# Performance work log

Hardware: AMD Instinct MI355X
Metric: run time of the kernel (lower is better)

The kernel has to match this reference:

```python
import jax, jax.numpy as jnp
import numpy as np

HEADS = 8
DIM_HEAD = 64
SCALE = DIM_HEAD ** -0.5
POS_DIM = 64


def _sincos_pe(H, W, dim, dtype):
    # matches build_2d_sincos_pos_embed: [1, dim, H, W]
    y = jnp.linspace(-1.0, 1.0, H)[:, None] * jnp.ones((1, W), jnp.float32)
    x = jnp.ones((H, 1), jnp.float32) * jnp.linspace(-1.0, 1.0, W)[None, :]
    omega = 1.0 / (10000.0 ** (jnp.arange(dim // 4, dtype=jnp.float32) / (dim // 4)))
    px = x[..., None] * omega  # [H, W, dim//4]
    py = y[..., None] * omega
    pe = jnp.concatenate([jnp.sin(px), jnp.cos(px), jnp.sin(py), jnp.cos(py)], axis=-1)
    return pe.transpose(2, 0, 1)[None].astype(dtype)


def _conv2d(x, w):
    return jax.lax.conv_general_dilated(
        x, w, (1, 1), 'SAME', dimension_numbers=('NCHW', 'OIHW', 'NCHW'))


def _sobel(d):
    kx = jnp.array([[1, 0, -1], [2, 0, -2], [1, 0, -1]], jnp.float32).reshape(1, 1, 3, 3)
    ky = jnp.array([[1, 2, 1], [0, 0, 0], [-1, -2, -1]], jnp.float32).reshape(1, 1, 3, 3)
    return _conv2d(d, kx), _conv2d(d, ky)


def setup_inputs() -> dict:
    key = jax.random.key(0)
    ks = jax.random.split(key, 8)
    B, C, H, W = 2, 256, 64, 64
    hid = HEADS * DIM_HEAD  # 512
    s = 0.02
    return {
        'x': jax.random.normal(ks[0], (B, C, H, W), jnp.float32),
        'dsm': jax.random.uniform(ks[1], (B, 1, H, W), jnp.float32),
        'wq': jax.random.normal(ks[2], (hid, C), jnp.float32) * s,
        'wkv': jax.random.normal(ks[3], (2 * hid, C + 1), jnp.float32) * s,
        'wout': jax.random.normal(ks[4], (C, hid), jnp.float32) * s,
        'bout': jnp.zeros((C,), jnp.float32),
        'w_hape': jax.random.normal(ks[5], (hid, POS_DIM + 3), jnp.float32) * s,
        'b_hape': jnp.zeros((hid,), jnp.float32),
        'w_alpha': jax.random.normal(ks[6], (1, 1, 3, 3), jnp.float32) * 0.1,
        'b_alpha': jnp.zeros((1,), jnp.float32),
    }


def reference(x, dsm, wq, wkv, wout, bout, w_hape, b_hape, w_alpha, b_alpha):
    B, C, H, W = x.shape
    hid = wq.shape[0]
    # per-sample min-max normalize DSM over spatial dims
    dmin = dsm.min(axis=(2, 3), keepdims=True)
    dmax = dsm.max(axis=(2, 3), keepdims=True)
    d = (dsm - dmin) / (dmax - dmin + 1e-6)
    # HAPE: [PE | h | grad_h] -> 1x1 conv to hidden
    pe = jnp.broadcast_to(_sincos_pe(H, W, POS_DIM, x.dtype), (B, POS_DIM, H, W))
    gx, gy = _sobel(d)
    hape_in = jnp.concatenate([pe, d, gx, gy], axis=1)  # [B, 67, H, W]
    hape_k = jnp.einsum('oc,bchw->bohw', w_hape, hape_in) + b_hape[None, :, None, None]
    # QKV via 1x1 convs
    q = jnp.einsum('oc,bchw->bohw', wq, x)
    kv = jnp.einsum('oc,bchw->bohw', wkv, jnp.concatenate([x, d], axis=1))
    k = kv[:, :hid] + hape_k
    v = kv[:, hid:]
    to_heads = lambda t: t.reshape(B, HEADS, DIM_HEAD, H * W)  # b (h c) x y -> b h c (xy)
    qh = to_heads(q) * SCALE
    kh = to_heads(k)
    vh = to_heads(v)
    sim = jnp.einsum('bhdi,bhdj->bhij', qh, kh)  # [B, h, N, N]
    attn = jax.nn.softmax(sim, axis=-1)
    out = jnp.einsum('bhij,bhdj->bhid', attn, vh)  # [B, h, N, d]
    # b h (x y) d -> b (h d) x y
    out = out.transpose(0, 1, 3, 2).reshape(B, HEADS * DIM_HEAD, H, W)
    out = jnp.einsum('oc,bchw->bohw', wout, out) + bout[None, :, None, None]
    # fine: gradient-magnitude alpha gating
    mag = jnp.sqrt(jnp.maximum(gx, 0.0) ** 2 + jnp.maximum(gy, 0.0) ** 2 + 1e-12)
    alpha = jax.nn.sigmoid(_conv2d(mag, w_alpha) + b_alpha[None, :, None, None])
    return x + out * alpha
```

## Files before the change

### kernel.cpp

```cpp
#include <hip/hip_runtime.h>
#include <math.h>

#define NPOS 4096
#define MTOT 8192
#define KP   352
#define HT 64
#define WT 64
#define NSPLIT 2
#define KEYS_PER (NPOS / NSPLIT)
#define NCH (KEYS_PER / 64)


typedef unsigned short ushortT;
typedef short v8s __attribute__((ext_vector_type(8)));
typedef float v4f __attribute__((ext_vector_type(4)));
typedef unsigned uint2v __attribute__((ext_vector_type(2)));

static __device__ __forceinline__ ushortT bfr(float f) {
    union { float f; unsigned u; } v; v.f = f;
    return (ushortT)((v.u + 0x8000u) >> 16);
}
static __device__ __forceinline__ unsigned pack2bf(float a, float b) {
    union { float f; unsigned u; } ua, ub; ua.f = a; ub.f = b;
    return __builtin_amdgcn_perm(ub.u + 0x8000u, ua.u + 0x8000u, 0x07060302u);
}
static __device__ __forceinline__ unsigned pack2bf_t(float a, float b) {
    union { float f; unsigned u; } ua, ub; ua.f = a; ub.f = b;
    return __builtin_amdgcn_perm(ub.u, ua.u, 0x07060302u);
}
static __device__ __forceinline__ float fexp2(float x) {
#if __has_builtin(__builtin_amdgcn_exp2f)
    return __builtin_amdgcn_exp2f(x);
#else
    return exp2f(x);
#endif
}
static __device__ __forceinline__ float bflo(unsigned u) {
    union { unsigned u; float f; } v; v.u = u << 16; return v.f;
}
static __device__ __forceinline__ float bfhi(unsigned u) {
    union { unsigned u; float f; } v; v.u = u & 0xffff0000u; return v.f;
}

__global__ void k_pre(const float* __restrict__ dsm,
                      const float* __restrict__ walpha, const float* __restrict__ balpha,
                      const float* __restrict__ x,
                      const float* __restrict__ wq, const float* __restrict__ wkv,
                      const float* __restrict__ whape, const float* __restrict__ bhape,
                      const float* __restrict__ wout,
                      ushortT* __restrict__ F, float* __restrict__ alpha,
                      ushortT* __restrict__ Wc, float* __restrict__ biasc,
                      ushortT* __restrict__ woutb) {
    __shared__ __align__(16) ushortT Tl[64][72];
    __shared__ float smn[4], smx[4];
    int role = blockIdx.x;
    int t = threadIdx.x;

    if (role < 32) {
        int idx = role * 256 + t;
        int b = idx / NPOS, n = idx % NPOS;
        int hh = n / WT, ww = n % WT;
        const float* dp = dsm + (size_t)b * NPOS;

        float mn = 1e30f, mx = -1e30f;
        for (int i = t; i < NPOS; i += 256) {
            float v = dp[i];
            mn = fminf(mn, v); mx = fmaxf(mx, v);
        }
        for (int off = 32; off; off >>= 1) {
            mn = fminf(mn, __shfl_xor(mn, off, 64));
            mx = fmaxf(mx, __shfl_xor(mx, off, 64));
        }
        int wid = t >> 6;
        if ((t & 63) == 0) { smn[wid] = mn; smx[wid] = mx; }
        __syncthreads();
        float dmin = fminf(fminf(smn[0], smn[1]), fminf(smn[2], smn[3]));
        float dmax = fmaxf(fmaxf(smx[0], smx[1]), fmaxf(smx[2], smx[3]));
        float inv = 1.0f / (dmax - dmin + 1e-6f);

        float dwin[5][5];
        #pragma unroll
        for (int dy = 0; dy < 5; dy++)
            #pragma unroll
            for (int dx = 0; dx < 5; dx++) {
                int y = hh + dy - 2, xx = ww + dx - 2;
                float v = 0.0f;
                if (y >= 0 && y < HT && xx >= 0 && xx < WT) v = (dp[y * WT + xx] - dmin) * inv;
                dwin[dy][dx] = v;
            }

        float gxc = 0.f, gyc = 0.f, conv = 0.f;
        #pragma unroll
        for (int oy = 0; oy < 3; oy++)
            #pragma unroll
            for (int ox = 0; ox < 3; ox++) {
                int qy = hh + oy - 1, qx = ww + ox - 1;
                float m = 0.0f;
                if (qy >= 0 && qy < HT && qx >= 0 && qx < WT) {
                    float gx = dwin[oy][ox] - dwin[oy][ox + 2]
                             + 2.f * dwin[oy + 1][ox] - 2.f * dwin[oy + 1][ox + 2]
                             + dwin[oy + 2][ox] - dwin[oy + 2][ox + 2];
                    float gy = dwin[oy][ox] + 2.f * dwin[oy][ox + 1] + dwin[oy][ox + 2]
                             - dwin[oy + 2][ox] - 2.f * dwin[oy + 2][ox + 1] - dwin[oy + 2][ox + 2];
                    if (oy == 1 && ox == 1) { gxc = gx; gyc = gy; }
                    float rx = fmaxf(gx, 0.f), ry = fmaxf(gy, 0.f);
                    m = sqrtf(rx * rx + ry * ry + 1e-12f);
                }
                conv += walpha[oy * 3 + ox] * m;
            }
        alpha[idx] = 1.f / (1.f + __expf(-(conv + balpha[0])));

        float xc = -1.f + 2.f * (float)ww / 63.f;
        float yc = -1.f + 2.f * (float)hh / 63.f;
        const float l2w = 13.287712379549449f;
        unsigned pe[32];
        #pragma unroll
        for (int i = 0; i < 16; i += 2) {
            float w0 = exp2f(-(float)i * (l2w / 16.f));
            float w1 = exp2f(-(float)(i + 1) * (l2w / 16.f));
            pe[i / 2]      = pack2bf(__sinf(xc * w0), __sinf(xc * w1));
            pe[8 + i / 2]  = pack2bf(__cosf(xc * w0), __cosf(xc * w1));
            pe[16 + i / 2] = pack2bf(__sinf(yc * w0), __sinf(yc * w1));
            pe[24 + i / 2] = pack2bf(__cosf(yc * w0), __cosf(yc * w1));
        }
        ushortT* fb = F + (size_t)idx * KP;
        uint4* dst = (uint4*)(fb + 256);
        #pragma unroll
        for (int q = 0; q < 8; q++) dst[q] = *(uint4*)&pe[q * 4];
        *(unsigned*)(fb + 320) = pack2bf(dwin[2][2], gxc);
        fb[322] = bfr(gyc);
        fb[323] = 0;
        *(unsigned*)(fb + 324) = 0;
        *(unsigned*)(fb + 326) = 0;
        uint4 z4 = {0, 0, 0, 0};
        *(uint4*)(fb + 328) = z4;
        *(uint4*)(fb + 336) = z4;
        *(uint4*)(fb + 344) = z4;
    } else if (role < 544) {
        int bid = role - 32;
        int nt = (bid & 63) * 64;
        int by = bid >> 6;
        int b = by >> 2, ct = (by & 3) * 64;
        #pragma unroll
        for (int rep = 0; rep < 4; rep++) {
            int row = rep * 16 + (t >> 4), c4 = (t & 15) * 4;
            float4 f4 = *(const float4*)&x[((size_t)(b * 256 + ct + row)) * NPOS + nt + c4];
            Tl[c4 + 0][row] = bfr(f4.x);
            Tl[c4 + 1][row] = bfr(f4.y);
            Tl[c4 + 2][row] = bfr(f4.z);
            Tl[c4 + 3][row] = bfr(f4.w);
        }
        __syncthreads();
        #pragma unroll
        for (int rep = 0; rep < 2; rep++) {
            int slot = rep * 256 + t, row = slot >> 3, c8 = slot & 7;
            *(uint4*)&F[((size_t)(b * 4096 + nt + row)) * KP + ct + c8 * 8] = *(uint4*)&Tl[row][c8 * 8];
        }
    } else {
        int bid = role - 544;
        int idx = bid * 256 + t;
        if (bid < 512) woutb[idx] = bfr(wout[idx]);
        int o = idx / KP, k = idx % KP;
        float v = 0.f;
        if (o < 512) {
            if (k < 256) v = wq[o * 256 + k] * 0.18033688011112042f;
            if (k == 0) biasc[o] = 0.f;
        } else if (o < 1024) {
            int r = o - 512;
            if (k < 256) v = wkv[r * 257 + k];
            else if (k < 320) v = whape[r * 67 + (k - 256)];
            else if (k == 320) v = wkv[r * 257 + 256] + whape[r * 67 + 64];
            else if (k == 321) v = whape[r * 67 + 65];
            else if (k == 322) v = whape[r * 67 + 66];
            if (k == 0) biasc[o] = bhape[r];
        } else {
            int r = o - 512;
            if (k < 256) v = wkv[r * 257 + k];
            else if (k == 320) v = wkv[r * 257 + 256];
            if (k == 0) biasc[o] = 0.f;
        }
        Wc[idx] = bfr(v);
    }
}

__global__ __launch_bounds__(256) void k_gemm1(const ushortT* __restrict__ Wc, const ushortT* __restrict__ F,
                                               const float* __restrict__ biasc,
                                               ushortT* __restrict__ qT, ushortT* __restrict__ kT,
                                               ushortT* __restrict__ vv) {
    __shared__ __align__(16) char smem[256 * 72 * 2];
    ushortT (*Al)[40] = (ushortT(*)[40])smem;
    ushortT (*Bl)[40] = (ushortT(*)[40])(smem + 20480);
    ushortT (*Vt)[72] = (ushortT(*)[72])smem;

    int mt = blockIdx.x * 64;
    int ot = blockIdx.y * 256;
    int t = threadIdx.x, w = t >> 6, lane = t & 63, u = lane & 15, quad = lane >> 4;
    v4f acc[4][4] = {};
    for (int k0 = 0; k0 < KP; k0 += 32) {
        __syncthreads();
        #pragma unroll
        for (int rep = 0; rep < 4; rep++) {
            int s = rep * 256 + t, row = s >> 2, ch = s & 3;
            *(uint4*)&Al[row][ch * 8] = *(const uint4*)&Wc[(size_t)(ot + row) * KP + k0 + ch * 8];
        }
        {
            int row = t >> 2, ch = t & 3;
            *(uint4*)&Bl[row][ch * 8] = *(const uint4*)&F[(size_t)(mt + row) * KP + k0 + ch * 8];
        }
        __syncthreads();
        v8s a[4], bb[4];
        #pragma unroll
        for (int rr = 0; rr < 4; rr++) a[rr] = *(v8s*)&Al[w * 64 + rr * 16 + u][quad * 8];
        #pragma unroll
        for (int n4 = 0; n4 < 4; n4++) bb[n4] = *(v8s*)&Bl[n4 * 16 + u][quad * 8];
        #pragma unroll
        for (int rr = 0; rr < 4; rr++)
            #pragma unroll
            for (int n4 = 0; n4 < 4; n4++)
                acc[rr][n4] = __builtin_amdgcn_mfma_f32_16x16x32_bf16(a[rr], bb[n4], acc[rr][n4], 0, 0, 0);
    }
    float bo[4][4];
    #pragma unroll
    for (int rr = 0; rr < 4; rr++)
        #pragma unroll
        for (int r = 0; r < 4; r++) bo[rr][r] = biasc[ot + w * 64 + rr * 16 + quad * 4 + r];
    if (ot < 1024) {
        ushortT* dst = (ot < 512) ? qT : kT;
        #pragma unroll
        for (int rr = 0; rr < 4; rr++) {
            int oo = ot + w * 64 + rr * 16;
            int h = (oo >> 6) & 7;
            int dcol = (oo & 63) + quad * 4;
            #pragma unroll
            for (int n4 = 0; n4 < 4; n4++) {
                int m = mt + n4 * 16 + u;
                uint2 val;
                val.x = pack2bf(acc[rr][n4][0] + bo[rr][0], acc[rr][n4][1] + bo[rr][1]);
                val.y = pack2bf(acc[rr][n4][2] + bo[rr][2], acc[rr][n4][3] + bo[rr][3]);
                *(uint2*)&dst[((size_t)h * MTOT + m) * 64 + dcol] = val;
            }
        }
    } else {
        __syncthreads();
        #pragma unroll
        for (int rr = 0; rr < 4; rr++)
            #pragma unroll
            for (int n4 = 0; n4 < 4; n4++) {
                int ml = n4 * 16 + u;
                #pragma unroll
                for (int r = 0; r < 4; r++)
                    Vt[w * 64 + rr * 16 + quad * 4 + r][ml] = bfr(acc[rr][n4][r] + bo[rr][r]);
            }
        __syncthreads();
        #pragma unroll
        for (int rep = 0; rep < 8; rep++) {
            int slot = rep * 256 + t, row = slot >> 3, c8 = slot & 7;
            *(uint4*)&vv[(size_t)(ot - 1024 + row) * MTOT + mt + c8 * 8] = *(uint4*)&Vt[row][c8 * 8];
        }
    }
}

#define LIDX(row, cb) (((row) << 6) + ((((cb) ^ ((row) & 7))) << 3))
__global__ __launch_bounds__(256, 4) void k_flash(const ushortT* __restrict__ qT,
                                                  const ushortT* __restrict__ kT,
                                                  const ushortT* __restrict__ vv,
                                                  ushortT* __restrict__ Opart,
                                                  float* __restrict__ liPart) {
    __shared__ __align__(16) ushortT Kbuf[2][64 * 64];
    __shared__ __align__(16) ushortT Vbuf[2][64 * 64];

    int it = blockIdx.x;
    int bh = blockIdx.y;
    int half = blockIdx.z;
    int b = bh >> 3, h = bh & 7;
    int colbase = b * NPOS;
    int t = threadIdx.x, w = t >> 6, lane = t & 63, u = lane & 15, quad = lane >> 4;
    int qb = it * 128 + w * 32;

    const ushortT* Qg = qT + ((size_t)h * MTOT + colbase + qb) * 64;
    const ushortT* Kg = kT + ((size_t)h * MTOT + colbase + half * KEYS_PER) * 64;
    const ushortT* Vg = vv + ((size_t)(h * 64)) * MTOT + colbase + half * KEYS_PER;

    int row0 = t >> 3, c80 = t & 7;
    int row1 = 32 + row0;

    unsigned boff[4][2];
    #pragma unroll
    for (int i4 = 0; i4 < 4; i4++) {
        boff[i4][0] = 2u * (unsigned)LIDX(i4 * 16 + u, quad);
        boff[i4][1] = 2u * (unsigned)LIDX(i4 * 16 + u, 4 + quad);
        asm volatile("" : "+v"(boff[i4][0]), "+v"(boff[i4][1]));
    }
    unsigned woff0 = 2u * (unsigned)LIDX(row0, c80);
    unsigned woff1 = 2u * (unsigned)LIDX(row1, c80);
    asm volatile("" : "+v"(woff0), "+v"(woff1));

    v8s bq[2][2];
    #pragma unroll
    for (int g = 0; g < 2; g++)
        #pragma unroll
        for (int hf = 0; hf < 2; hf++)
            bq[g][hf] = *(const v8s*)&Qg[(size_t)(g * 16 + u) * 64 + hf * 32 + quad * 8];

    v8s ones;
    #pragma unroll
    for (int i = 0; i < 8; i++) ones[i] = (short)0x3F80;

    v4f li4[2] = {};
    v4f O[4][2] = {};

    uint4 kr0 = *(const uint4*)&Kg[(size_t)row0 * 64 + c80 * 8];
    uint4 kr1 = *(const uint4*)&Kg[(size_t)row1 * 64 + c80 * 8];
    uint4 vr0 = *(const uint4*)&Vg[(size_t)row0 * MTOT + c80 * 8];
    uint4 vr1 = *(const uint4*)&Vg[(size_t)row1 * MTOT + c80 * 8];

    #pragma unroll 2
    for (int jc = 0; jc < NCH; jc++) {
        int cur = jc & 1;
        char* KbW = (char*)&Kbuf[cur][0];
        char* VbW = (char*)&Vbuf[cur][0];
        *(uint4*)(KbW + woff0) = kr0;
        *(uint4*)(KbW + woff1) = kr1;
        *(uint4*)(VbW + woff0) = vr0;
        *(uint4*)(VbW + woff1) = vr1;
        __syncthreads();
        if (jc + 1 < NCH) {
            int jb = (jc + 1) * 64;
            kr0 = *(const uint4*)&Kg[(size_t)(jb + row0) * 64 + c80 * 8];
            kr1 = *(const uint4*)&Kg[(size_t)(jb + row1) * 64 + c80 * 8];
            vr0 = *(const uint4*)&Vg[(size_t)row0 * MTOT + jb + c80 * 8];
            vr1 = *(const uint4*)&Vg[(size_t)row1 * MTOT + jb + c80 * 8];
        }

        const char* Kb = (const char*)&Kbuf[cur][0];
        const char* Vb = (const char*)&Vbuf[cur][0];

        v8s bp[2][2];
        #pragma unroll
        for (int kp = 0; kp < 2; kp++) {
            unsigned pk0[2][2], pk1[2][2];
            #pragma unroll
            for (int kk = 0; kk < 2; kk++) {
                int k4 = kp * 2 + kk;
                v8s ak0 = *(const v8s*)(Kb + boff[k4][0]);
                v8s ak1 = *(const v8s*)(Kb + boff[k4][1]);
                v4f st[2];
                __builtin_amdgcn_s_setprio(1);
                #pragma unroll
                for (int g = 0; g < 2; g++) {
                    st[g] = (v4f){0.f, 0.f, 0.f, 0.f};
                    st[g] = __builtin_amdgcn_mfma_f32_16x16x32_bf16(ak0, bq[g][0], st[g], 0, 0, 0);
                    st[g] = __builtin_amdgcn_mfma_f32_16x16x32_bf16(ak1, bq[g][1], st[g], 0, 0, 0);
                }
                __builtin_amdgcn_s_setprio(0);
                #pragma unroll
                for (int g = 0; g < 2; g++) {
                    float p0 = fexp2(st[g][0]);
                    float p1 = fexp2(st[g][1]);
                    float p2 = fexp2(st[g][2]);
                    float p3 = fexp2(st[g][3]);
                    pk0[g][kk] = pack2bf_t(p0, p1);
                    pk1[g][kk] = pack2bf_t(p2, p3);
                }
            }
            #pragma unroll
            for (int g = 0; g < 2; g++) {
                uint2v r0s = __builtin_amdgcn_permlane32_swap(pk0[g][0], pk0[g][1], false, false);
                uint2v r1s = __builtin_amdgcn_permlane32_swap(pk1[g][0], pk1[g][1], false, false);
                uint2v t0 = __builtin_amdgcn_permlane16_swap(r0s.x, r0s.y, false, false);
                uint2v t1 = __builtin_amdgcn_permlane16_swap(r1s.x, r1s.y, false, false);
                union { uint4 u4; v8s s; } cv;
                cv.u4.x = t0.x; cv.u4.y = t1.x; cv.u4.z = t0.y; cv.u4.w = t1.y;
                bp[g][kp] = cv.s;
            }
        }

        __builtin_amdgcn_s_setprio(1);
        #pragma unroll
        for (int g = 0; g < 2; g++) {
            li4[g] = __builtin_amdgcn_mfma_f32_16x16x32_bf16(ones, bp[g][0], li4[g], 0, 0, 0);
            li4[g] = __builtin_amdgcn_mfma_f32_16x16x32_bf16(ones, bp[g][1], li4[g], 0, 0, 0);
        }
        #pragma unroll
        for (int d4 = 0; d4 < 4; d4++) {
            v8s av0 = *(const v8s*)(Vb + boff[d4][0]);
            v8s av1 = *(const v8s*)(Vb + boff[d4][1]);
            #pragma unroll
            for (int g = 0; g < 2; g++) {
                O[d4][g] = __builtin_amdgcn_mfma_f32_16x16x32_bf16(av0, bp[g][0], O[d4][g], 0, 0, 0);
                O[d4][g] = __builtin_amdgcn_mfma_f32_16x16x32_bf16(av1, bp[g][1], O[d4][g], 0, 0, 0);
            }
        }
        __builtin_amdgcn_s_setprio(0);
    }

    #pragma unroll
    for (int g = 0; g < 2; g++) {
        int q = qb + g * 16 + u;
        size_t m2 = (size_t)(half * 2 + b) * 4096 + q;
        size_t base = m2 * 512 + h * 64;
        #pragma unroll
        for (int d4 = 0; d4 < 4; d4++) {
            uint2 o2;
            o2.x = pack2bf(O[d4][g][0], O[d4][g][1]);
            o2.y = pack2bf(O[d4][g][2], O[d4][g][3]);
            *(uint2*)&Opart[base + d4 * 16 + quad * 4] = o2;
        }
        if (quad == 0) liPart[m2 * 8 + h] = li4[g][0];
    }
}

__global__ __launch_bounds__(256) void k_comb(const ushortT* __restrict__ Opart,
                                              const float* __restrict__ liPart,
                                              ushortT* __restrict__ aoB) {
    int tid = blockIdx.x * 256 + threadIdx.x;
    int m = tid >> 7, c4 = (tid & 127) * 4, h = c4 >> 6;
    float l = 0.f;
    #pragma unroll
    for (int s = 0; s < NSPLIT; s++) l += liPart[((size_t)s * 8192 + m) * 8 + h];
    float inv = 1.f / l;
    float ox = 0.f, oy = 0.f, oz = 0.f, ow = 0.f;
    #pragma unroll
    for (int s = 0; s < NSPLIT; s++) {
        uint2 o = *(const uint2*)&Opart[((size_t)s * 8192 + m) * 512 + c4];
        ox += bflo(o.x); oy += bfhi(o.x);
        oz += bflo(o.y); ow += bfhi(o.y);
    }
    uint2 val;
    val.x = pack2bf(ox * inv, oy * inv);
    val.y = pack2bf(oz * inv, ow * inv);
    *(uint2*)&aoB[(size_t)m * 512 + c4] = val;
}

__global__ __launch_bounds__(256) void k_gemm2(const ushortT* __restrict__ woutb, const ushortT* __restrict__ aoB,
                                               const float* __restrict__ bout, const float* __restrict__ x,
                                               const float* __restrict__ alpha, float* __restrict__ out) {
    __shared__ __align__(16) ushortT Al[64][40];
    __shared__ __align__(16) ushortT Bl[64][40];
    int mt = blockIdx.x * 64;
    int ot = blockIdx.y * 64;
    int t = threadIdx.x, w = t >> 6, lane = t & 63, u = lane & 15, quad = lane >> 4;
    int arow = t >> 2, ac8 = t & 3;
    v4f acc[4] = {};
    for (int k0 = 0; k0 < 512; k0 += 32) {
        __syncthreads();
        *(uint4*)&Al[arow][ac8 * 8] = *(const uint4*)&woutb[(size_t)(ot + arow) * 512 + k0 + ac8 * 8];
        *(uint4*)&Bl[arow][ac8 * 8] = *(const uint4*)&aoB[(size_t)(mt + arow) * 512 + k0 + ac8 * 8];
        __syncthreads();
        v8s a = *(v8s*)&Al[w * 16 + u][quad * 8];
        #pragma unroll
        for (int n4 = 0; n4 < 4; n4++) {
            v8s bb = *(v8s*)&Bl[n4 * 16 + u][quad * 8];
            acc[n4] = __builtin_amdgcn_mfma_f32_16x16x32_bf16(a, bb, acc[n4], 0, 0, 0);
        }
    }
    int b = mt >> 12, n0 = mt & 4095;
    int obase = ot + w * 16 + quad * 4;
    float bo[4];
    #pragma unroll
    for (int r = 0; r < 4; r++) bo[r] = bout[obase + r];
    #pragma unroll
    for (int n4 = 0; n4 < 4; n4++) {
        int n = n0 + n4 * 16 + u;
        float al = alpha[(size_t)b * NPOS + n];
        #pragma unroll
        for (int r = 0; r < 4; r++) {
            size_t xi = ((size_t)(b * 256 + obase + r)) * NPOS + n;
            out[xi] = x[xi] + (acc[n4][r] + bo[r]) * al;
        }
    }
}

extern "C" void kernel_launch(void* const* d_in, const int* in_sizes, int n_in,
                              void* d_out, int out_size, void* d_ws, size_t ws_size,
                              hipStream_t stream) {
    const float* x      = (const float*)d_in[0];
    const float* dsm    = (const float*)d_in[1];
    const float* wq     = (const float*)d_in[2];
    const float* wkv    = (const float*)d_in[3];
    const float* wout   = (const float*)d_in[4];
    const float* bout   = (const float*)d_in[5];
    const float* whape  = (const float*)d_in[6];
    const float* bhape  = (const float*)d_in[7];
    const float* walpha = (const float*)d_in[8];
    const float* balpha = (const float*)d_in[9];
    float* out = (float*)d_out;
    float* ws  = (float*)d_ws;

    size_t off = 0;
    float* alpha = ws + off; off += (size_t)2 * NPOS;
    float* biasc = ws + off; off += 2048;
    float* liPart = ws + off; off += (size_t)NSPLIT * MTOT * 8;
    ushortT* Opart = (ushortT*)(ws + off); off += (size_t)NSPLIT * MTOT * 512 / 2;
    ushortT* F     = (ushortT*)(ws + off); off += (size_t)MTOT * KP / 2;
    ushortT* Wc    = (ushortT*)(ws + off); off += (size_t)1536 * KP / 2;
    ushortT* woutb = (ushortT*)(ws + off); off += (size_t)256 * 512 / 2;
    ushortT* qT    = (ushortT*)(ws + off); off += (size_t)8 * MTOT * 64 / 2;
    ushortT* kT    = (ushortT*)(ws + off); off += (size_t)8 * MTOT * 64 / 2;
    ushortT* vv    = (ushortT*)(ws + off); off += (size_t)512 * MTOT / 2;
    ushortT* aoB   = (ushortT*)(ws + off); off += (size_t)MTOT * 512 / 2;
    (void)in_sizes; (void)n_in; (void)out_size; (void)ws_size;

    k_pre<<<2656, 256, 0, stream>>>(dsm, walpha, balpha, x, wq, wkv, whape, bhape, wout,
                                    F, alpha, Wc, biasc, woutb);
    k_gemm1<<<dim3(128, 6), 256, 0, stream>>>(Wc, F, biasc, qT, kT, vv);
    k_flash<<<dim3(32, 16, NSPLIT), 256, 0, stream>>>(qT, kT, vv, Opart, liPart);
    k_comb<<<4096, 256, 0, stream>>>(Opart, liPart, aoB);
    k_gemm2<<<dim3(128, 4), 256, 0, stream>>>(woutb, aoB, bout, x, alpha, out);
}
```

Baseline: 201.5 us.

## Fuse split-KV combine into output GEMM and register-prefetch GEMM tiles

Removes the separate combine kernel by merging the two split-KV partial outputs and normalizing by the summed row sums inside the output projection GEMM while staging the B tile. This drops one launch and the round trip of the combined attention output through global memory. Both GEMMs now prefetch the next K-slice into registers while the current slice is being multiplied. The output GEMM also uses 128-row output tiles, which halves the grid. The combine work is now repeated in each of the two output-tile column blocks.

New measurement: 198.4 us. No clear change (-1.6%).

```diff
diff --git a/kernel.cpp b/kernel.cpp
--- a/kernel.cpp
+++ b/kernel.cpp
@@ -195,19 +195,35 @@
     int mt = blockIdx.x * 64;
     int ot = blockIdx.y * 256;
     int t = threadIdx.x, w = t >> 6, lane = t & 63, u = lane & 15, quad = lane >> 4;
+    int r4 = t >> 2, ch = t & 3;
+
+    const ushortT* pA0 = Wc + (size_t)(ot +   0 + r4) * KP + ch * 8;
+    const ushortT* pA1 = Wc + (size_t)(ot +  64 + r4) * KP + ch * 8;
+    const ushortT* pA2 = Wc + (size_t)(ot + 128 + r4) * KP + ch * 8;
+    const ushortT* pA3 = Wc + (size_t)(ot + 192 + r4) * KP + ch * 8;
+    const ushortT* pB  = F  + (size_t)(mt + r4) * KP + ch * 8;
+    uint4 ra0 = *(const uint4*)pA0;
+    uint4 ra1 = *(const uint4*)pA1;
+    uint4 ra2 = *(const uint4*)pA2;
+    uint4 ra3 = *(const uint4*)pA3;
+    uint4 rb  = *(const uint4*)pB;
+
     v4f acc[4][4] = {};
     for (int k0 = 0; k0 < KP; k0 += 32) {
-        __syncthreads();
-        #pragma unroll
-        for (int rep = 0; rep < 4; rep++) {
-            int s = rep * 256 + t, row = s >> 2, ch = s & 3;
-            *(uint4*)&Al[row][ch * 8] = *(const uint4*)&Wc[(size_t)(ot + row) * KP + k0 + ch * 8];
-        }
-        {
-            int row = t >> 2, ch = t & 3;
-            *(uint4*)&Bl[row][ch * 8] = *(const uint4*)&F[(size_t)(mt + row) * KP + k0 + ch * 8];
-        }
-        __syncthreads();
+        *(uint4*)&Al[  0 + r4][ch * 8] = ra0;
+        *(uint4*)&Al[ 64 + r4][ch * 8] = ra1;
+        *(uint4*)&Al[128 + r4][ch * 8] = ra2;
+        *(uint4*)&Al[192 + r4][ch * 8] = ra3;
+        *(uint4*)&Bl[r4][ch * 8] = rb;
+        __syncthreads();
+        if (k0 + 32 < KP) {
+            pA0 += 32; pA1 += 32; pA2 += 32; pA3 += 32; pB += 32;
+            ra0 = *(const uint4*)pA0;
+            ra1 = *(const uint4*)pA1;
+            ra2 = *(const uint4*)pA2;
+            ra3 = *(const uint4*)pA3;
+            rb  = *(const uint4*)pB;
+        }
         v8s a[4], bb[4];
         #pragma unroll
         for (int rr = 0; rr < 4; rr++) a[rr] = *(v8s*)&Al[w * 64 + rr * 16 + u][quad * 8];
@@ -218,6 +234,7 @@
             #pragma unroll
             for (int n4 = 0; n4 < 4; n4++)
                 acc[rr][n4] = __builtin_amdgcn_mfma_f32_16x16x32_bf16(a[rr], bb[n4], acc[rr][n4], 0, 0, 0);
+        __syncthreads();
     }
     float bo[4][4];
     #pragma unroll
@@ -241,7 +258,6 @@
             }
         }
     } else {
-        __syncthreads();
         #pragma unroll
         for (int rr = 0; rr < 4; rr++)
             #pragma unroll
@@ -410,63 +426,81 @@
     }
 }
 
-__global__ __launch_bounds__(256) void k_comb(const ushortT* __restrict__ Opart,
-                                              const float* __restrict__ liPart,
-                                              ushortT* __restrict__ aoB) {
-    int tid = blockIdx.x * 256 + threadIdx.x;
-    int m = tid >> 7, c4 = (tid & 127) * 4, h = c4 >> 6;
-    float l = 0.f;
-    #pragma unroll
-    for (int s = 0; s < NSPLIT; s++) l += liPart[((size_t)s * 8192 + m) * 8 + h];
-    float inv = 1.f / l;
-    float ox = 0.f, oy = 0.f, oz = 0.f, ow = 0.f;
-    #pragma unroll
-    for (int s = 0; s < NSPLIT; s++) {
-        uint2 o = *(const uint2*)&Opart[((size_t)s * 8192 + m) * 512 + c4];
-        ox += bflo(o.x); oy += bfhi(o.x);
-        oz += bflo(o.y); ow += bfhi(o.y);
-    }
-    uint2 val;
-    val.x = pack2bf(ox * inv, oy * inv);
-    val.y = pack2bf(oz * inv, ow * inv);
-    *(uint2*)&aoB[(size_t)m * 512 + c4] = val;
-}
-
-__global__ __launch_bounds__(256) void k_gemm2(const ushortT* __restrict__ woutb, const ushortT* __restrict__ aoB,
+__global__ __launch_bounds__(256) void k_gemm2(const ushortT* __restrict__ woutb,
+                                               const ushortT* __restrict__ Opart,
+                                               const float* __restrict__ liPart,
                                                const float* __restrict__ bout, const float* __restrict__ x,
                                                const float* __restrict__ alpha, float* __restrict__ out) {
-    __shared__ __align__(16) ushortT Al[64][40];
+    __shared__ __align__(16) ushortT Al[128][40];
     __shared__ __align__(16) ushortT Bl[64][40];
     int mt = blockIdx.x * 64;
-    int ot = blockIdx.y * 64;
+    int ot = blockIdx.y * 128;
     int t = threadIdx.x, w = t >> 6, lane = t & 63, u = lane & 15, quad = lane >> 4;
-    int arow = t >> 2, ac8 = t & 3;
-    v4f acc[4] = {};
+    int r4 = t >> 2, ch = t & 3;
+    int m = mt + r4;
+
+    float linv[8];
+    #pragma unroll
+    for (int h = 0; h < 8; h++)
+        linv[h] = 1.f / (liPart[(size_t)m * 8 + h] + liPart[(size_t)(8192 + m) * 8 + h]);
+
+    const ushortT* pA0 = woutb + (size_t)(ot + r4) * 512 + ch * 8;
+    const ushortT* pA1 = woutb + (size_t)(ot + 64 + r4) * 512 + ch * 8;
+    const ushortT* pO0 = Opart + (size_t)m * 512 + ch * 8;
+    const ushortT* pO1 = Opart + (size_t)(8192 + m) * 512 + ch * 8;
+    uint4 ra0 = *(const uint4*)pA0;
+    uint4 ra1 = *(const uint4*)pA1;
+    uint4 ro0 = *(const uint4*)pO0;
+    uint4 ro1 = *(const uint4*)pO1;
+
+    v4f acc[2][4] = {};
     for (int k0 = 0; k0 < 512; k0 += 32) {
-        __syncthreads();
-        *(uint4*)&Al[arow][ac8 * 8] = *(const uint4*)&woutb[(size_t)(ot + arow) * 512 + k0 + ac8 * 8];
-        *(uint4*)&Bl[arow][ac8 * 8] = *(const uint4*)&aoB[(size_t)(mt + arow) * 512 + k0 + ac8 * 8];
-        __syncthreads();
-        v8s a = *(v8s*)&Al[w * 16 + u][quad * 8];
+        int h = (k0 + ch * 8) >> 6;
+        float iv = linv[h];
+        uint4 bv;
+        bv.x = pack2bf((bflo(ro0.x) + bflo(ro1.x)) * iv, (bfhi(ro0.x) + bfhi(ro1.x)) * iv);
+        bv.y = pack2bf((bflo(ro0.y) + bflo(ro1.y)) * iv, (bfhi(ro0.y) + bfhi(ro1.y)) * iv);
+        bv.z = pack2bf((bflo(ro0.z) + bflo(ro1.z)) * iv, (bfhi(ro0.z) + bfhi(ro1.z)) * iv);
+        bv.w = pack2bf((bflo(ro0.w) + bflo(ro1.w)) * iv, (bfhi(ro0.w) + bfhi(ro1.w)) * iv);
+        *(uint4*)&Al[r4][ch * 8] = ra0;
+        *(uint4*)&Al[64 + r4][ch * 8] = ra1;
+        *(uint4*)&Bl[r4][ch * 8] = bv;
+        __syncthreads();
+        if (k0 + 32 < 512) {
+            pA0 += 32; pA1 += 32; pO0 += 32; pO1 += 32;
+            ra0 = *(const uint4*)pA0;
+            ra1 = *(const uint4*)pA1;
+            ro0 = *(const uint4*)pO0;
+            ro1 = *(const uint4*)pO1;
+        }
+        v8s a[2], bb[4];
+        #pragma unroll
+        for (int rr = 0; rr < 2; rr++) a[rr] = *(v8s*)&Al[w * 32 + rr * 16 + u][quad * 8];
+        #pragma unroll
+        for (int n4 = 0; n4 < 4; n4++) bb[n4] = *(v8s*)&Bl[n4 * 16 + u][quad * 8];
+        #pragma unroll
+        for (int rr = 0; rr < 2; rr++)
+            #pragma unroll
+            for (int n4 = 0; n4 < 4; n4++)
+                acc[rr][n4] = __builtin_amdgcn_mfma_f32_16x16x32_bf16(a[rr], bb[n4], acc[rr][n4], 0, 0, 0);
+        __syncthreads();
+    }
+    int b = mt >> 12, n0 = mt & 4095;
+    #pragma unroll
+    for (int rr = 0; rr < 2; rr++) {
+        int obase = ot + w * 32 + rr * 16 + quad * 4;
+        float bo[4];
+        #pragma unroll
+        for (int r = 0; r < 4; r++) bo[r] = bout[obase + r];
         #pragma unroll
         for (int n4 = 0; n4 < 4; n4++) {
-            v8s bb = *(v8s*)&Bl[n4 * 16 + u][quad * 8];
-            acc[n4] = __builtin_amdgcn_mfma_f32_16x16x32_bf16(a, bb, acc[n4], 0, 0, 0);
-        }
-    }
-    int b = mt >> 12, n0 = mt & 4095;
-    int obase = ot + w * 16 + quad * 4;
-    float bo[4];
-    #pragma unroll
-    for (int r = 0; r < 4; r++) bo[r] = bout[obase + r];
-    #pragma unroll
-    for (int n4 = 0; n4 < 4; n4++) {
-        int n = n0 + n4 * 16 + u;
-        float al = alpha[(size_t)b * NPOS + n];
-        #pragma unroll
-        for (int r = 0; r < 4; r++) {
-            size_t xi = ((size_t)(b * 256 + obase + r)) * NPOS + n;
-            out[xi] = x[xi] + (acc[n4][r] + bo[r]) * al;
+            int n = n0 + n4 * 16 + u;
+            float al = alpha[(size_t)b * NPOS + n];
+            #pragma unroll
+            for (int r = 0; r < 4; r++) {
+                size_t xi = ((size_t)(b * 256 + obase + r)) * NPOS + n;
+                out[xi] = x[xi] + (acc[rr][n4][r] + bo[r]) * al;
+            }
         }
     }
 }
@@ -498,13 +532,11 @@
     ushortT* qT    = (ushortT*)(ws + off); off += (size_t)8 * MTOT * 64 / 2;
     ushortT* kT    = (ushortT*)(ws + off); off += (size_t)8 * MTOT * 64 / 2;
     ushortT* vv    = (ushortT*)(ws + off); off += (size_t)512 * MTOT / 2;
-    ushortT* aoB   = (ushortT*)(ws + off); off += (size_t)MTOT * 512 / 2;
     (void)in_sizes; (void)n_in; (void)out_size; (void)ws_size;
 
     k_pre<<<2656, 256, 0, stream>>>(dsm, walpha, balpha, x, wq, wkv, whape, bhape, wout,
                                     F, alpha, Wc, biasc, woutb);
     k_gemm1<<<dim3(128, 6), 256, 0, stream>>>(Wc, F, biasc, qT, kT, vv);
     k_flash<<<dim3(32, 16, NSPLIT), 256, 0, stream>>>(qT, kT, vv, Opart, liPart);
-    k_comb<<<4096, 256, 0, stream>>>(Opart, liPart, aoB);
-    k_gemm2<<<dim3(128, 4), 256, 0, stream>>>(woutb, aoB, bout, x, alpha, out);
-}
+    k_gemm2<<<dim3(128, 2), 256, 0, stream>>>(woutb, Opart, liPart, bout, x, alpha, out);
+}
```
